# Kernel tuning notes

Measured on AMD Instinct MI355X. Metric: run time of the kernel, lower is better.

## Reference

```python
import jax, jax.numpy as jnp
import numpy as np

B, S, D = 4, 2048, 1024
H = 16
HD = D // H  # 64


def _xavier(key, shape):
    fan_in, fan_out = shape[1], shape[0]
    limit = float(np.sqrt(6.0 / (fan_in + fan_out)))
    return jax.random.uniform(key, shape, jnp.float32, -limit, limit)


def setup_inputs() -> dict:
    key = jax.random.key(0)
    ks = jax.random.split(key, 5)
    x = jax.random.normal(ks[0], (B, S, D), dtype=jnp.float32)
    # nn.Linear weights are [out, in]; biases zero-initialized
    Wq = _xavier(ks[1], (D, D)); bq = jnp.zeros((D,), jnp.float32)
    Wk = _xavier(ks[2], (D, D)); bk = jnp.zeros((D,), jnp.float32)
    Wv = _xavier(ks[3], (D, D)); bv = jnp.zeros((D,), jnp.float32)
    Wo = _xavier(ks[4], (D, D)); bo = jnp.zeros((D,), jnp.float32)
    return {"x": x, "Wq": Wq, "bq": bq, "Wk": Wk, "bk": bk,
            "Wv": Wv, "bv": bv, "Wo": Wo, "bo": bo}


def reference(x, Wq, bq, Wk, bk, Wv, bv, Wo, bo):
    # Projections (torch Linear: y = x @ W.T + b), reshape to [B, H, S, HD]
    def proj(W, b):
        y = jnp.einsum('bsd,ed->bse', x, W) + b
        return y.reshape(B, S, H, HD).transpose(0, 2, 1, 3)

    q = proj(Wq, bq)
    k = proj(Wk, bk)
    v = proj(Wv, bv)

    scale = 1.0 / jnp.sqrt(jnp.float32(HD))
    scores = jnp.einsum('bhqd,bhkd->bhqk', q, k) * scale  # [B,H,S,S]
    probs = jax.nn.softmax(scores, axis=-1)
    ctx = jnp.einsum('bhqk,bhkd->bhqd', probs, v)  # [B,H,S,HD]
    ctx = ctx.transpose(0, 2, 1, 3).reshape(B, S, D)
    out = jnp.einsum('bsd,ed->bse', ctx, Wo) + bo
    return out
```

## Files before the change

### kernel.cpp

```cpp
#include <hip/hip_runtime.h>
#include <hip/hip_bf16.h>
#include <stdint.h>


typedef __bf16 bf16;
typedef __bf16 bf16x8 __attribute__((ext_vector_type(8)));
typedef __bf16 bf16x4 __attribute__((ext_vector_type(4)));
typedef float  f32x4  __attribute__((ext_vector_type(4)));

#define MFMA_BF16(A, B, C) __builtin_amdgcn_mfma_f32_16x16x32_bf16(A, B, C, 0, 0, 0)
#define EXP2F(x) __builtin_amdgcn_exp2f(x)

#define ASYNC_CP16(DST_LDS, SRC_G)                                            \
  __builtin_amdgcn_global_load_lds(                                           \
      (__attribute__((address_space(1))) void*)(SRC_G),                       \
      (__attribute__((address_space(3))) void*)(DST_LDS), 16, 0, 0)

__global__ __launch_bounds__(256) void cvt5(
    const float* __restrict__ s0, bf16* __restrict__ d0, int n0,
    const float* __restrict__ s1, bf16* __restrict__ d1, int n1,
    const float* __restrict__ s2, bf16* __restrict__ d2, int n2,
    const float* __restrict__ s3, bf16* __restrict__ d3, int n3,
    const float* __restrict__ s4, bf16* __restrict__ d4, int n4)
{
  const float* s; bf16* d; int n;
  switch (blockIdx.y) {
    case 0: s = s0; d = d0; n = n0; break;
    case 1: s = s1; d = d1; n = n1; break;
    case 2: s = s2; d = d2; n = n2; break;
    case 3: s = s3; d = d3; n = n3; break;
    default: s = s4; d = d4; n = n4; break;
  }
  const int stride = gridDim.x * blockDim.x * 4;
  for (int i = (blockIdx.x * blockDim.x + threadIdx.x) * 4; i < n; i += stride) {
    const float4 v = *(const float4*)(s + i);
    bf16x4 o;
    o[0] = (bf16)v.x; o[1] = (bf16)v.y; o[2] = (bf16)v.z; o[3] = (bf16)v.w;
    *(bf16x4*)(d + i) = o;
  }
}

__global__ __launch_bounds__(256) void gemm_bt(
    const bf16* __restrict__ X, const bf16* __restrict__ W,
    const float* __restrict__ bias, bf16* __restrict__ Yb,
    float* __restrict__ Yf, int M, int N, int K, int mode, float scale)
{
  __shared__ alignas(16) bf16 As[8192];
  __shared__ alignas(16) bf16 Bs[8192];

  const int tid  = threadIdx.x;
  const int lane = tid & 63;
  const int wv   = tid >> 6;
  const int l15  = lane & 15;
  const int quad = lane >> 4;
  const int wm   = (wv >> 1) * 64;
  const int wn   = (wv & 1) * 64;
  const int nbase = blockIdx.x * 128;
  const int mbase = blockIdx.y * 128;

  f32x4 acc[4][4];
  #pragma unroll
  for (int i = 0; i < 4; ++i)
    #pragma unroll
    for (int j = 0; j < 4; ++j)
      acc[i][j] = (f32x4){0.f, 0.f, 0.f, 0.f};

  const int r8 = lane >> 3;
  const int oc = (lane & 7) ^ r8;
  const size_t lrowA = (size_t)(mbase + wv * 32 + r8);
  const size_t lrowB = (size_t)(nbase + wv * 32 + r8);

  for (int kb = 0; kb < K; kb += 64) {
    #pragma unroll
    for (int c = 0; c < 4; ++c) {
      const bf16* gA = X + (lrowA + c * 8) * K + kb + oc * 8;
      ASYNC_CP16(As + (wv * 32 + c * 8) * 64, gA);
      const bf16* gB = W + (lrowB + c * 8) * K + kb + oc * 8;
      ASYNC_CP16(Bs + (wv * 32 + c * 8) * 64, gB);
    }
    __syncthreads();
    #pragma unroll
    for (int ks = 0; ks < 2; ++ks) {
      bf16x8 af[4], bfr[4];
      #pragma unroll
      for (int t = 0; t < 4; ++t) {
        const int ma = wm + t * 16 + l15;
        af[t]  = *(const bf16x8*)(As + (ma * 8 + ((ks * 4 + quad) ^ (ma & 7))) * 8);
        const int nb = wn + t * 16 + l15;
        bfr[t] = *(const bf16x8*)(Bs + (nb * 8 + ((ks * 4 + quad) ^ (nb & 7))) * 8);
      }
      #pragma unroll
      for (int i = 0; i < 4; ++i)
        #pragma unroll
        for (int j = 0; j < 4; ++j)
          acc[i][j] = MFMA_BF16(af[i], bfr[j], acc[i][j]);
    }
    __syncthreads();
  }

  #pragma unroll
  for (int i = 0; i < 4; ++i) {
    const int row0 = mbase + wm + i * 16 + quad * 4;
    #pragma unroll
    for (int j = 0; j < 4; ++j) {
      const int col = nbase + wn + j * 16 + l15;
      const float bv = bias[col];
      #pragma unroll
      for (int r = 0; r < 4; ++r) {
        const float v = (acc[i][j][r] + bv) * scale;
        const int row = row0 + r;
        if (mode == 0) {
          Yb[(size_t)row * N + col] = (bf16)v;
        } else if (mode == 1) {
          const int bb = row >> 11, s  = row & 2047;
          const int hh = col >> 6,  hd = col & 63;
          Yb[(size_t)((bb * 16 + hh) * 64 + hd) * 2048 + s] = (bf16)v;
        } else {
          Yf[(size_t)row * N + col] = v;
        }
      }
    }
  }
}

__global__ __launch_bounds__(256, 2) void attn(
    const bf16* __restrict__ Qb, const bf16* __restrict__ Kb,
    const bf16* __restrict__ Vt, bf16* __restrict__ Ob)
{
  constexpr int S = 2048, D = 1024;
  __shared__ alignas(16) bf16 Ks[2][4096];
  __shared__ alignas(16) bf16 Vs[2][4096];

  const int tid  = threadIdx.x;
  const int lane = tid & 63;
  const int wv   = tid >> 6;
  const int l15  = lane & 15;
  const int q0   = lane >> 4;
  const int b = blockIdx.z, h = blockIdx.y;
  const int qblk = blockIdx.x * 256 + wv * 64;

  bf16x8 qf[4][2];
  #pragma unroll
  for (int qt = 0; qt < 4; ++qt)
    #pragma unroll
    for (int dh = 0; dh < 2; ++dh)
      qf[qt][dh] = *(const bf16x8*)(
          Qb + (size_t)(b * S + qblk + qt * 16 + l15) * D + h * 64 + dh * 32 + q0 * 8);

  float mrun[4], lrun[4];
  f32x4 o[4][4];
  #pragma unroll
  for (int qt = 0; qt < 4; ++qt) { mrun[qt] = -__builtin_inff(); lrun[qt] = 0.f; }
  #pragma unroll
  for (int ht = 0; ht < 4; ++ht)
    #pragma unroll
    for (int qt = 0; qt < 4; ++qt)
      o[ht][qt] = (f32x4){0.f, 0.f, 0.f, 0.f};

  const int skey = lane;
  const int so   = wv;
  const bf16* kg = Kb + (size_t)(b * S) * D + h * 64;
  const bf16* vg = Vt + (size_t)((b * 16 + h) * 64) * S;
  const int swk = (skey & 3) | (((skey >> 3) & 1) << 2);

  const int kla = 8 * (l15 >> 2) + (l15 & 3);
  const int swa = (l15 & 3) | (((l15 >> 2) & 1) << 2);
  const int swv = l15 & 7;

#define STAGE(KC, BUF)                                                        \
  {                                                                           \
    const bf16* krow = kg + (size_t)((KC) + skey) * D;                        \
    const bf16x8 k0 = *(const bf16x8*)(krow + so * 8);                        \
    const bf16x8 k1 = *(const bf16x8*)(krow + (so + 4) * 8);                  \
    *(bf16x8*)(&Ks[BUF][(skey * 8 + (so ^ swk)) * 8]) = k0;                   \
    *(bf16x8*)(&Ks[BUF][(skey * 8 + ((so + 4) ^ swk)) * 8]) = k1;             \
    const bf16* vrow = vg + (size_t)skey * S + (KC);                          \
    const bf16x8 v0 = *(const bf16x8*)(vrow + so * 8);                        \
    const bf16x8 v1 = *(const bf16x8*)(vrow + (so + 4) * 8);                  \
    *(bf16x8*)(&Vs[BUF][(skey * 8 + (so ^ (skey & 7))) * 8]) = v0;            \
    *(bf16x8*)(&Vs[BUF][(skey * 8 + ((so + 4) ^ (skey & 7))) * 8]) = v1;      \
  }

  STAGE(0, 0);

  for (int kc = 0, it = 0; kc < S; kc += 64, ++it) {
    const int cur = it & 1;
    __syncthreads();
    if (kc + 64 < S) STAGE(kc + 64, cur ^ 1);

    f32x4 sc[4][4];
    #pragma unroll
    for (int kt = 0; kt < 4; ++kt) {
      const int key = kla + 4 * (kt & 1) + 32 * (kt >> 1);
      const bf16x8 kf0 = *(const bf16x8*)(&Ks[cur][(key * 8 + (q0 ^ swa)) * 8]);
      const bf16x8 kf1 = *(const bf16x8*)(&Ks[cur][(key * 8 + ((q0 + 4) ^ swa)) * 8]);
      #pragma unroll
      for (int qt = 0; qt < 4; ++qt) {
        f32x4 s = MFMA_BF16(kf0, qf[qt][0], ((f32x4){0.f, 0.f, 0.f, 0.f}));
        sc[qt][kt] = MFMA_BF16(kf1, qf[qt][1], s);
      }
    }

    bf16x8 pb[4][2];
    #pragma unroll
    for (int qt = 0; qt < 4; ++qt) {
      float cmax = sc[qt][0][0];
      #pragma unroll
      for (int kt = 0; kt < 4; ++kt)
        #pragma unroll
        for (int r = 0; r < 4; ++r)
          cmax = fmaxf(cmax, sc[qt][kt][r]);
      cmax = fmaxf(cmax, __shfl_xor(cmax, 16, 64));
      cmax = fmaxf(cmax, __shfl_xor(cmax, 32, 64));
      const float mnew  = fmaxf(mrun[qt], cmax);
      const float alpha = EXP2F(mrun[qt] - mnew);
      mrun[qt] = mnew;
      float ps = 0.f;
      #pragma unroll
      for (int kt = 0; kt < 4; ++kt)
        #pragma unroll
        for (int r = 0; r < 4; ++r) {
          const float p = EXP2F(sc[qt][kt][r] - mnew);
          ps += p;
          pb[qt][kt >> 1][(kt & 1) * 4 + r] = (bf16)p;
        }
      lrun[qt] = lrun[qt] * alpha + ps;
      #pragma unroll
      for (int ht = 0; ht < 4; ++ht) {
        o[ht][qt][0] *= alpha; o[ht][qt][1] *= alpha;
        o[ht][qt][2] *= alpha; o[ht][qt][3] *= alpha;
      }
    }

    #pragma unroll
    for (int ht = 0; ht < 4; ++ht) {
      const int row = ht * 16 + l15;
      const bf16x8 vf0 = *(const bf16x8*)(&Vs[cur][(row * 8 + (q0 ^ swv)) * 8]);
      const bf16x8 vf1 = *(const bf16x8*)(&Vs[cur][(row * 8 + ((q0 + 4) ^ swv)) * 8]);
      #pragma unroll
      for (int qt = 0; qt < 4; ++qt) {
        o[ht][qt] = MFMA_BF16(vf0, pb[qt][0], o[ht][qt]);
        o[ht][qt] = MFMA_BF16(vf1, pb[qt][1], o[ht][qt]);
      }
    }
  }
#undef STAGE

  #pragma unroll
  for (int qt = 0; qt < 4; ++qt) {
    float l = lrun[qt];
    l += __shfl_xor(l, 16, 64);
    l += __shfl_xor(l, 32, 64);
    const float inv = 1.0f / l;
    bf16* orow = Ob + (size_t)(b * S + qblk + qt * 16 + l15) * D + h * 64 + q0 * 4;
    #pragma unroll
    for (int ht = 0; ht < 4; ++ht) {
      bf16x4 w;
      w[0] = (bf16)(o[ht][qt][0] * inv);
      w[1] = (bf16)(o[ht][qt][1] * inv);
      w[2] = (bf16)(o[ht][qt][2] * inv);
      w[3] = (bf16)(o[ht][qt][3] * inv);
      *(bf16x4*)(orow + ht * 16) = w;
    }
  }
}

extern "C" void kernel_launch(void* const* d_in, const int* in_sizes, int n_in,
                              void* d_out, int out_size, void* d_ws, size_t ws_size,
                              hipStream_t stream)
{
  const float* x  = (const float*)d_in[0];
  const float* Wq = (const float*)d_in[1];
  const float* bq = (const float*)d_in[2];
  const float* Wk = (const float*)d_in[3];
  const float* bk = (const float*)d_in[4];
  const float* Wv = (const float*)d_in[5];
  const float* bv = (const float*)d_in[6];
  const float* Wo = (const float*)d_in[7];
  const float* bo = (const float*)d_in[8];
  float* out = (float*)d_out;

  const size_t NX = (size_t)8192 * 1024;
  const size_t NW = (size_t)1024 * 1024;

  bf16* xb  = (bf16*)d_ws;
  bf16* Wqb = xb  + NX;
  bf16* Wkb = Wqb + NW;
  bf16* Wvb = Wkb + NW;
  bf16* Wob = Wvb + NW;
  bf16* Qb  = Wob + NW;
  bf16* Kb  = Qb  + NX;
  bf16* Vt  = Kb  + NX;
  bf16* Ctx = Vt  + NX;

  const float QSCALE = 0.18033688011112042f;

  dim3 bc(256, 1, 1);
  hipLaunchKernelGGL(cvt5, dim3(1024, 5, 1), bc, 0, stream,
                     x, xb, (int)NX, Wq, Wqb, (int)NW, Wk, Wkb, (int)NW,
                     Wv, Wvb, (int)NW, Wo, Wob, (int)NW);

  dim3 gg(8, 64, 1);
  hipLaunchKernelGGL(gemm_bt, gg, bc, 0, stream, xb, Wqb, bq, Qb, (float*)nullptr, 8192, 1024, 1024, 0, QSCALE);
  hipLaunchKernelGGL(gemm_bt, gg, bc, 0, stream, xb, Wkb, bk, Kb, (float*)nullptr, 8192, 1024, 1024, 0, 1.0f);
  hipLaunchKernelGGL(gemm_bt, gg, bc, 0, stream, xb, Wvb, bv, Vt, (float*)nullptr, 8192, 1024, 1024, 1, 1.0f);
  dim3 ga(8, 16, 4);
  hipLaunchKernelGGL(attn, ga, bc, 0, stream, Qb, Kb, Vt, Ctx);
  hipLaunchKernelGGL(gemm_bt, gg, bc, 0, stream, Ctx, Wob, bo, (bf16*)nullptr, out, 8192, 1024, 1024, 2, 1.0f);
}
```

Baseline: 336.3 us.

## Merge QKV projections into one launch and halve attention query tile per block

The three Q/K/V projection GEMMs become a single kernel launch with a 24x64 grid, where the block index selects the weight, bias and output layout. The attention kernel now handles 128 queries per block (32 per wave) instead of 256, doubling the grid to 1024 blocks, and raises launch bounds to 4 blocks per CU to improve occupancy and latency hiding. The output GEMM is reduced to a plain fp32 path with no mode branches. Smaller query tiles mean each K/V tile loaded into LDS is reused across fewer queries, so K/V traffic per unit of work doubles.

```diff
diff --git a/kernel.cpp b/kernel.cpp
--- a/kernel.cpp
+++ b/kernel.cpp
@@ -40,10 +40,100 @@
   }
 }
 
+__global__ __launch_bounds__(256, 4) void gemm_qkv(
+    const bf16* __restrict__ X,
+    const bf16* __restrict__ Wq, const bf16* __restrict__ Wk,
+    const bf16* __restrict__ Wv,
+    const float* __restrict__ bq, const float* __restrict__ bk,
+    const float* __restrict__ bv,
+    bf16* __restrict__ Qo, bf16* __restrict__ Ko, bf16* __restrict__ Vo,
+    float qscale)
+{
+  constexpr int N = 1024, K = 1024;
+  __shared__ alignas(16) bf16 As[8192];
+  __shared__ alignas(16) bf16 Bs[8192];
+
+  const int sel = blockIdx.x >> 3;
+  const bf16*  W    = (sel == 0) ? Wq : (sel == 1) ? Wk : Wv;
+  const float* bias = (sel == 0) ? bq : (sel == 1) ? bk : bv;
+  bf16*        Y    = (sel == 0) ? Qo : (sel == 1) ? Ko : Vo;
+  const float scale = (sel == 0) ? qscale : 1.0f;
+
+  const int tid  = threadIdx.x;
+  const int lane = tid & 63;
+  const int wv   = tid >> 6;
+  const int l15  = lane & 15;
+  const int quad = lane >> 4;
+  const int wm   = (wv >> 1) * 64;
+  const int wn   = (wv & 1) * 64;
+  const int nbase = (blockIdx.x & 7) * 128;
+  const int mbase = blockIdx.y * 128;
+
+  f32x4 acc[4][4];
+  #pragma unroll
+  for (int i = 0; i < 4; ++i)
+    #pragma unroll
+    for (int j = 0; j < 4; ++j)
+      acc[i][j] = (f32x4){0.f, 0.f, 0.f, 0.f};
+
+  const int r8 = lane >> 3;
+  const int oc = (lane & 7) ^ r8;
+  const size_t lrowA = (size_t)(mbase + wv * 32 + r8);
+  const size_t lrowB = (size_t)(nbase + wv * 32 + r8);
+
+  for (int kb = 0; kb < K; kb += 64) {
+    #pragma unroll
+    for (int c = 0; c < 4; ++c) {
+      ASYNC_CP16(As + (wv * 32 + c * 8) * 64, X + (lrowA + c * 8) * K + kb + oc * 8);
+      ASYNC_CP16(Bs + (wv * 32 + c * 8) * 64, W + (lrowB + c * 8) * K + kb + oc * 8);
+    }
+    __syncthreads();
+    #pragma unroll
+    for (int ks = 0; ks < 2; ++ks) {
+      bf16x8 af[4], bfr[4];
+      #pragma unroll
+      for (int t = 0; t < 4; ++t) {
+        const int ma = wm + t * 16 + l15;
+        af[t]  = *(const bf16x8*)(As + (ma * 8 + ((ks * 4 + quad) ^ (ma & 7))) * 8);
+        const int nb = wn + t * 16 + l15;
+        bfr[t] = *(const bf16x8*)(Bs + (nb * 8 + ((ks * 4 + quad) ^ (nb & 7))) * 8);
+      }
+      #pragma unroll
+      for (int i = 0; i < 4; ++i)
+        #pragma unroll
+        for (int j = 0; j < 4; ++j)
+          acc[i][j] = MFMA_BF16(af[i], bfr[j], acc[i][j]);
+    }
+    __syncthreads();
+  }
+
+  #pragma unroll
+  for (int i = 0; i < 4; ++i) {
+    const int row0 = mbase + wm + i * 16 + quad * 4;
+    #pragma unroll
+    for (int j = 0; j < 4; ++j) {
+      const int col = nbase + wn + j * 16 + l15;
+      const float bv2 = bias[col];
+      #pragma unroll
+      for (int r = 0; r < 4; ++r) {
+        const float v = (acc[i][j][r] + bv2) * scale;
+        const int row = row0 + r;
+        if (sel != 2) {
+          Y[(size_t)row * N + col] = (bf16)v;
+        } else {
+          const int bb = row >> 11, s  = row & 2047;
+          const int hh = col >> 6,  hd = col & 63;
+          Y[(size_t)((bb * 16 + hh) * 64 + hd) * 2048 + s] = (bf16)v;
+        }
+      }
+    }
+  }
+}
+
 __global__ __launch_bounds__(256) void gemm_bt(
     const bf16* __restrict__ X, const bf16* __restrict__ W,
-    const float* __restrict__ bias, bf16* __restrict__ Yb,
-    float* __restrict__ Yf, int M, int N, int K, int mode, float scale)
+    const float* __restrict__ bias, float* __restrict__ Yf,
+    int M, int N, int K)
 {
   __shared__ alignas(16) bf16 As[8192];
   __shared__ alignas(16) bf16 Bs[8192];
@@ -73,10 +163,8 @@
   for (int kb = 0; kb < K; kb += 64) {
     #pragma unroll
     for (int c = 0; c < 4; ++c) {
-      const bf16* gA = X + (lrowA + c * 8) * K + kb + oc * 8;
-      ASYNC_CP16(As + (wv * 32 + c * 8) * 64, gA);
-      const bf16* gB = W + (lrowB + c * 8) * K + kb + oc * 8;
-      ASYNC_CP16(Bs + (wv * 32 + c * 8) * 64, gB);
+      ASYNC_CP16(As + (wv * 32 + c * 8) * 64, X + (lrowA + c * 8) * K + kb + oc * 8);
+      ASYNC_CP16(Bs + (wv * 32 + c * 8) * 64, W + (lrowB + c * 8) * K + kb + oc * 8);
     }
     __syncthreads();
     #pragma unroll
@@ -104,26 +192,15 @@
     #pragma unroll
     for (int j = 0; j < 4; ++j) {
       const int col = nbase + wn + j * 16 + l15;
-      const float bv = bias[col];
-      #pragma unroll
-      for (int r = 0; r < 4; ++r) {
-        const float v = (acc[i][j][r] + bv) * scale;
-        const int row = row0 + r;
-        if (mode == 0) {
-          Yb[(size_t)row * N + col] = (bf16)v;
-        } else if (mode == 1) {
-          const int bb = row >> 11, s  = row & 2047;
-          const int hh = col >> 6,  hd = col & 63;
-          Yb[(size_t)((bb * 16 + hh) * 64 + hd) * 2048 + s] = (bf16)v;
-        } else {
-          Yf[(size_t)row * N + col] = v;
-        }
-      }
-    }
-  }
-}
-
-__global__ __launch_bounds__(256, 2) void attn(
+      const float bv2 = bias[col];
+      #pragma unroll
+      for (int r = 0; r < 4; ++r)
+        Yf[(size_t)(row0 + r) * N + col] = acc[i][j][r] + bv2;
+    }
+  }
+}
+
+__global__ __launch_bounds__(256, 4) void attn(
     const bf16* __restrict__ Qb, const bf16* __restrict__ Kb,
     const bf16* __restrict__ Vt, bf16* __restrict__ Ob)
 {
@@ -137,24 +214,24 @@
   const int l15  = lane & 15;
   const int q0   = lane >> 4;
   const int b = blockIdx.z, h = blockIdx.y;
-  const int qblk = blockIdx.x * 256 + wv * 64;
-
-  bf16x8 qf[4][2];
-  #pragma unroll
-  for (int qt = 0; qt < 4; ++qt)
+  const int qblk = blockIdx.x * 128 + wv * 32;
+
+  bf16x8 qf[2][2];
+  #pragma unroll
+  for (int qt = 0; qt < 2; ++qt)
     #pragma unroll
     for (int dh = 0; dh < 2; ++dh)
       qf[qt][dh] = *(const bf16x8*)(
           Qb + (size_t)(b * S + qblk + qt * 16 + l15) * D + h * 64 + dh * 32 + q0 * 8);
 
-  float mrun[4], lrun[4];
-  f32x4 o[4][4];
-  #pragma unroll
-  for (int qt = 0; qt < 4; ++qt) { mrun[qt] = -__builtin_inff(); lrun[qt] = 0.f; }
+  float mrun[2], lrun[2];
+  f32x4 o[4][2];
+  #pragma unroll
+  for (int qt = 0; qt < 2; ++qt) { mrun[qt] = -__builtin_inff(); lrun[qt] = 0.f; }
   #pragma unroll
   for (int ht = 0; ht < 4; ++ht)
     #pragma unroll
-    for (int qt = 0; qt < 4; ++qt)
+    for (int qt = 0; qt < 2; ++qt)
       o[ht][qt] = (f32x4){0.f, 0.f, 0.f, 0.f};
 
   const int skey = lane;
@@ -188,22 +265,22 @@
     __syncthreads();
     if (kc + 64 < S) STAGE(kc + 64, cur ^ 1);
 
-    f32x4 sc[4][4];
+    f32x4 sc[2][4];
     #pragma unroll
     for (int kt = 0; kt < 4; ++kt) {
       const int key = kla + 4 * (kt & 1) + 32 * (kt >> 1);
       const bf16x8 kf0 = *(const bf16x8*)(&Ks[cur][(key * 8 + (q0 ^ swa)) * 8]);
       const bf16x8 kf1 = *(const bf16x8*)(&Ks[cur][(key * 8 + ((q0 + 4) ^ swa)) * 8]);
       #pragma unroll
-      for (int qt = 0; qt < 4; ++qt) {
+      for (int qt = 0; qt < 2; ++qt) {
         f32x4 s = MFMA_BF16(kf0, qf[qt][0], ((f32x4){0.f, 0.f, 0.f, 0.f}));
         sc[qt][kt] = MFMA_BF16(kf1, qf[qt][1], s);
       }
     }
 
-    bf16x8 pb[4][2];
-    #pragma unroll
-    for (int qt = 0; qt < 4; ++qt) {
+    bf16x8 pb[2][2];
+    #pragma unroll
+    for (int qt = 0; qt < 2; ++qt) {
       float cmax = sc[qt][0][0];
       #pragma unroll
       for (int kt = 0; kt < 4; ++kt)
@@ -238,7 +315,7 @@
       const bf16x8 vf0 = *(const bf16x8*)(&Vs[cur][(row * 8 + (q0 ^ swv)) * 8]);
       const bf16x8 vf1 = *(const bf16x8*)(&Vs[cur][(row * 8 + ((q0 + 4) ^ swv)) * 8]);
       #pragma unroll
-      for (int qt = 0; qt < 4; ++qt) {
+      for (int qt = 0; qt < 2; ++qt) {
         o[ht][qt] = MFMA_BF16(vf0, pb[qt][0], o[ht][qt]);
         o[ht][qt] = MFMA_BF16(vf1, pb[qt][1], o[ht][qt]);
       }
@@ -247,7 +324,7 @@
 #undef STAGE
 
   #pragma unroll
-  for (int qt = 0; qt < 4; ++qt) {
+  for (int qt = 0; qt < 2; ++qt) {
     float l = lrun[qt];
     l += __shfl_xor(l, 16, 64);
     l += __shfl_xor(l, 32, 64);
@@ -300,11 +377,11 @@
                      x, xb, (int)NX, Wq, Wqb, (int)NW, Wk, Wkb, (int)NW,
                      Wv, Wvb, (int)NW, Wo, Wob, (int)NW);
 
-  dim3 gg(8, 64, 1);
-  hipLaunchKernelGGL(gemm_bt, gg, bc, 0, stream, xb, Wqb, bq, Qb, (float*)nullptr, 8192, 1024, 1024, 0, QSCALE);
-  hipLaunchKernelGGL(gemm_bt, gg, bc, 0, stream, xb, Wkb, bk, Kb, (float*)nullptr, 8192, 1024, 1024, 0, 1.0f);
-  hipLaunchKernelGGL(gemm_bt, gg, bc, 0, stream, xb, Wvb, bv, Vt, (float*)nullptr, 8192, 1024, 1024, 1, 1.0f);
-  dim3 ga(8, 16, 4);
-  hipLaunchKernelGGL(attn, ga, bc, 0, stream, Qb, Kb, Vt, Ctx);
-  hipLaunchKernelGGL(gemm_bt, gg, bc, 0, stream, Ctx, Wob, bo, (bf16*)nullptr, out, 8192, 1024, 1024, 2, 1.0f);
-}
+  hipLaunchKernelGGL(gemm_qkv, dim3(24, 64, 1), bc, 0, stream,
+                     xb, Wqb, Wkb, Wvb, bq, bk, bv, Qb, Kb, Vt, QSCALE);
+
+  hipLaunchKernelGGL(attn, dim3(16, 16, 4), bc, 0, stream, Qb, Kb, Vt, Ctx);
+
+  hipLaunchKernelGGL(gemm_bt, dim3(8, 64, 1), bc, 0, stream,
+                     Ctx, Wob, bo, out, 8192, 1024, 1024);
+}
```

After: 300.1 us. -10.8%, faster.
